# Optimization experiments

Measured on AMD Instinct MI355X. Metric: run time of the kernel, lower is better.

The kernel has to match this reference:

```python
import jax, jax.numpy as jnp
import numpy as np

DIM = 1024          # hidden_size
HEADS = 16
KDIM = DIM // 2     # expand_k = 0.5
VDIM = DIM          # expand_v = 1.0
DK = KDIM // HEADS  # 32 head key dim
DV = VDIM // HEADS  # 64 head value dim
LOW = 16            # gate_low_rank_dim
NORMALIZER = 16.0   # gate_logit_normalizer
EPS = 1e-5
B, T = 2, 4096


def setup_inputs() -> dict:
    key = jax.random.key(0)
    ks = jax.random.split(key, 9)
    def lin(k, sh, fan_in):
        return jax.random.normal(k, sh, jnp.float32) * (fan_in ** -0.5)
    return {
        "x":    jax.random.normal(ks[0], (B, T, DIM), jnp.float32),
        "Wq":   lin(ks[1], (DIM, KDIM), DIM),
        "Wk":   lin(ks[2], (DIM, KDIM), DIM),
        "Wv":   lin(ks[3], (DIM, VDIM), DIM),
        "Wgk1": lin(ks[4], (DIM, LOW), DIM),   # low-rank gate proj (no bias)
        "Wgk2": lin(ks[5], (LOW, KDIM), LOW),  # low-rank gate proj (with bias)
        "bgk2": jnp.zeros((KDIM,), jnp.float32),
        "Wg":   lin(ks[6], (DIM, VDIM), DIM),  # output gate proj (no bias)
        "gnw":  jnp.ones((DV,), jnp.float32),  # per-head RMSNorm weight
        "Wo":   lin(ks[7], (VDIM, DIM), VDIM),
    }


def _gla_scan(q, k, v, gk):
    # q,k,gk: (B,T,H,DK)  v: (B,T,H,DV)
    # recurrent form of chunked GLA: h_t = exp(gk_t) (x) h_{t-1} + k_t (outer) v_t
    scale = DK ** -0.5
    def step(h, inp):
        qt, kt, vt, gt = inp                      # (B,H,DK)/(B,H,DV)
        h = h * jnp.exp(gt)[..., None] + kt[..., None] * vt[..., None, :]
        ot = jnp.einsum('bhk,bhkv->bhv', qt * scale, h)
        return h, ot
    h0 = jnp.zeros((q.shape[0], HEADS, DK, DV), q.dtype)
    xs = tuple(jnp.moveaxis(a, 1, 0) for a in (q, k, v, gk))  # time-major
    _, o = jax.lax.scan(step, h0, xs)
    return jnp.moveaxis(o, 0, 1)                  # (B,T,H,DV)


def reference(x, Wq, Wk, Wv, Wgk1, Wgk2, bgk2, Wg, gnw, Wo):
    Bx, Tx, _ = x.shape
    q = (x @ Wq).reshape(Bx, Tx, HEADS, DK)
    k = (x @ Wk).reshape(Bx, Tx, HEADS, DK)
    v = (x @ Wv).reshape(Bx, Tx, HEADS, DV)
    # data-dependent log-decay gate: logsigmoid(low-rank proj) / normalizer
    gk = jax.nn.log_sigmoid((x @ Wgk1) @ Wgk2 + bgk2)
    gk = gk.reshape(Bx, Tx, HEADS, DK) / NORMALIZER
    o = _gla_scan(q, k, v, gk)                    # (B,T,H,DV)
    # fused per-head RMSNorm + swish output gate
    g = (x @ Wg).reshape(Bx, Tx, HEADS, DV)
    o = o * jax.lax.rsqrt(jnp.mean(o * o, axis=-1, keepdims=True) + EPS) * gnw
    o = o * (g * jax.nn.sigmoid(g))
    return o.reshape(Bx, Tx, VDIM) @ Wo
```

## Files before the change

### kernel.cpp

```cpp
#include <hip/hip_runtime.h>

typedef unsigned short u16;
typedef unsigned int u32;
typedef __attribute__((ext_vector_type(8))) short short8;
typedef __attribute__((ext_vector_type(4))) float f32x4;

#define KD 512
#define HEADS 16
#define DK 32
#define DV 64
#define TT 4096
#define MROWS 8192
#define CHUNK 64
#define NCH 64
#define NBH 32
#define QSTR 3328
#define SCALE 0.17677669529663687f

__device__ __forceinline__ u16 f2bf(float f) {
    union { float f; unsigned int u; } x; x.f = f;
    unsigned int u = x.u;
    unsigned int r = (u + 0x7fffu + ((u >> 16) & 1u)) >> 16;
    return (u16)r;
}
__device__ __forceinline__ float bf2f(u16 s) {
    union { unsigned int u; float f; } x; x.u = ((unsigned int)s) << 16;
    return x.f;
}
__device__ __forceinline__ void gload16(const u16* g, u16* l) {
    __builtin_amdgcn_global_load_lds((const __attribute__((address_space(1))) u32*)g,
                                     (__attribute__((address_space(3))) u32*)l, 16, 0, 0);
}

__global__ __launch_bounds__(256) void f32_to_bf16_vec(const float* __restrict__ src,
                                                       u16* __restrict__ dst, int n4) {
    int i = blockIdx.x * 256 + threadIdx.x;
    if (i < n4) {
        const float4 v = ((const float4*)src)[i];
        ushort4 o;
        o.x = f2bf(v.x); o.y = f2bf(v.y); o.z = f2bf(v.z); o.w = f2bf(v.w);
        ((ushort4*)dst)[i] = o;
    }
}

__global__ __launch_bounds__(256) void weight_prep(const float* __restrict__ Wq,
                                                   const float* __restrict__ Wk,
                                                   const float* __restrict__ Wv,
                                                   const float* __restrict__ Wg,
                                                   const float* __restrict__ W1,
                                                   const float* __restrict__ Wo,
                                                   u16* __restrict__ dst) {
    __shared__ float tile[32][33];
    int n0 = blockIdx.x * 32, k0 = blockIdx.y * 32;
    int tx = threadIdx.x & 31, ty = threadIdx.x >> 5;
    int n = n0 + tx;
    const float* src; int sN, cc;
    if (n < 512)       { src = Wq; sN = 512;  cc = n; }
    else if (n < 1024) { src = Wk; sN = 512;  cc = n - 512; }
    else if (n < 2048) { src = Wv; sN = 1024; cc = n - 1024; }
    else if (n < 3072) { src = Wg; sN = 1024; cc = n - 2048; }
    else if (n < 3088) { src = W1; sN = 16;   cc = n - 3072; }
    else if (n < 3328) { src = nullptr; sN = 0; cc = 0; }
    else               { src = Wo; sN = 1024; cc = n - 3328; }
    for (int r = ty; r < 32; r += 8)
        tile[r][tx] = src ? src[(size_t)(k0 + r) * sN + cc] : 0.f;
    __syncthreads();
    for (int r = ty; r < 32; r += 8)
        dst[(size_t)(n0 + r) * 1024 + k0 + tx] = f2bf(tile[tx][r]);
}

#define BARM() do { asm volatile("" ::: "memory"); __builtin_amdgcn_s_barrier(); asm volatile("" ::: "memory"); } while (0)
#define VMW(n) asm volatile("s_waitcnt vmcnt(" #n ")" ::: "memory")

template<int OUTBF>
__global__ __launch_bounds__(512, 2) void gemm8(const u16* __restrict__ A,
                                                const u16* __restrict__ Bt,
                                                void* __restrict__ C,
                                                int M, int N, int K, int nbx) {
    __shared__ u16 SA[2][16384];
    __shared__ u16 SB[2][16384];
    int nwg = gridDim.x, bid = blockIdx.x, cpx = nwg >> 3;
    int wg = (bid & 7) * cpx + (bid >> 3);
    int bx = wg % nbx, by = wg / nbx;
    int brow = by << 8, bcol = bx << 8;
    int tid = threadIdx.x;
    int wv = tid >> 6, lane = tid & 63;
    int wm = wv >> 2, wn = wv & 3;
    int l15 = lane & 15, hi = lane >> 4;
    int rxor = l15 & 7;

    int srw = tid >> 3;
    int sg8 = ((tid & 7) ^ (srw & 7)) << 3;
    const u16* aBase = A + (size_t)(brow + srw) * K + sg8;
    const u16* bBase = Bt + (size_t)(bcol + ((tid >> 8) << 6) + (srw & 31)) * K + sg8;

#define STAGE_A(b, h, tt) do { \
        const u16* s_ = aBase + (size_t)(tt) * 64 + (size_t)(h) * 64 * K; \
        gload16(s_,                    &SA[b][(h) * 8192 + tid * 8]); \
        gload16(s_ + (size_t)128 * K,  &SA[b][(h) * 8192 + 4096 + tid * 8]); \
    } while (0)
#define STAGE_B(b, h, tt) do { \
        const u16* s_ = bBase + (size_t)(tt) * 64 + (size_t)(h) * 32 * K; \
        gload16(s_,                    &SB[b][(h) * 8192 + tid * 8]); \
        gload16(s_ + (size_t)128 * K,  &SB[b][(h) * 8192 + 4096 + tid * 8]); \
    } while (0)

    int aRow = (wm * 64 + l15) * 64;
    int bRow = (wn * 32 + l15) * 64;
    int cg0 = (hi ^ rxor) << 3;
    int cg1 = ((4 + hi) ^ rxor) << 3;

#define READ_A(dst, mh, b) do { \
        _Pragma("unroll") \
        for (int mil_ = 0; mil_ < 4; ++mil_) { \
            dst[mil_ * 2 + 0] = *(const short8*)&SA[b][(mh) * 8192 + mil_ * 1024 + aRow + cg0]; \
            dst[mil_ * 2 + 1] = *(const short8*)&SA[b][(mh) * 8192 + mil_ * 1024 + aRow + cg1]; \
        } } while (0)
#define READ_B(dst, nh, b) do { \
        _Pragma("unroll") \
        for (int nil_ = 0; nil_ < 2; ++nil_) { \
            dst[nil_ * 2 + 0] = *(const short8*)&SB[b][(nh) * 8192 + nil_ * 1024 + bRow + cg0]; \
            dst[nil_ * 2 + 1] = *(const short8*)&SB[b][(nh) * 8192 + nil_ * 1024 + bRow + cg1]; \
        } } while (0)

    f32x4 acc[8][4];
    #pragma unroll
    for (int mi = 0; mi < 8; ++mi)
        #pragma unroll
        for (int ni = 0; ni < 4; ++ni)
            acc[mi][ni] = (f32x4){0.f, 0.f, 0.f, 0.f};

#define MM(mb, nb, AF, BF) do { \
        __builtin_amdgcn_s_setprio(1); \
        _Pragma("unroll") \
        for (int ks_ = 0; ks_ < 2; ++ks_) \
        _Pragma("unroll") \
        for (int mil_ = 0; mil_ < 4; ++mil_) \
        _Pragma("unroll") \
        for (int nil_ = 0; nil_ < 2; ++nil_) \
            acc[(mb) + mil_][(nb) + nil_] = __builtin_amdgcn_mfma_f32_16x16x32_bf16( \
                AF[mil_ * 2 + ks_], BF[nil_ * 2 + ks_], acc[(mb) + mil_][(nb) + nil_], 0, 0, 0); \
        __builtin_amdgcn_s_setprio(0); \
    } while (0)

    int NK = K >> 6, NI = NK >> 1;
    STAGE_B(0, 0, 0); STAGE_A(0, 0, 0); STAGE_A(0, 1, 0); STAGE_B(0, 1, 0);
    STAGE_B(1, 0, 1); STAGE_A(1, 0, 1); STAGE_A(1, 1, 1);
    VMW(6);
    BARM();

    short8 alo[8], ahi[8], bb[4];
    for (int i = 0; i < NI; ++i) {
        int ta = 2 * i + 1; if (ta >= NK) ta = NK - 1;
        int tb = 2 * i + 2; if (tb >= NK) tb = NK - 1;
        int tc = 2 * i + 3; if (tc >= NK) tc = NK - 1;
        STAGE_B(1, 1, ta);
        READ_A(alo, 0, 0); READ_B(bb, 0, 0);
        BARM(); MM(0, 0, alo, bb); BARM();
        STAGE_B(0, 0, tb);
        READ_A(ahi, 1, 0);
        BARM(); MM(4, 0, ahi, bb); BARM();
        STAGE_A(0, 0, tb); STAGE_A(0, 1, tb);
        READ_B(bb, 1, 0);
        BARM(); MM(4, 2, ahi, bb); MM(0, 2, alo, bb);
        VMW(8);
        BARM();
        STAGE_B(0, 1, tb);
        READ_A(alo, 0, 1); READ_B(bb, 0, 1);
        BARM(); MM(0, 0, alo, bb); BARM();
        STAGE_B(1, 0, tc);
        READ_A(ahi, 1, 1);
        BARM(); MM(4, 0, ahi, bb);
        VMW(10);
        BARM();
        STAGE_A(1, 0, tc); STAGE_A(1, 1, tc);
        READ_B(bb, 1, 1);
        BARM(); MM(4, 2, ahi, bb); MM(0, 2, alo, bb);
        VMW(6);
        BARM();
    }

    int r0 = brow + wm * 128 + (hi << 2);
    int c0 = bcol + wn * 64 + l15;
    #pragma unroll
    for (int mi = 0; mi < 8; ++mi)
        #pragma unroll
        for (int ni = 0; ni < 4; ++ni)
            #pragma unroll
            for (int rr = 0; rr < 4; ++rr) {
                size_t idx = (size_t)(r0 + mi * 16 + rr) * N + (c0 + ni * 16);
                float val = acc[mi][ni][rr];
                if (OUTBF) ((u16*)C)[idx] = f2bf(val);
                else       ((float*)C)[idx] = val;
            }
#undef STAGE_A
#undef STAGE_B
#undef READ_A
#undef READ_B
#undef MM
}

template<int OUTBF>
__global__ __launch_bounds__(256) void gemm_sb(const u16* __restrict__ A,
                                               const u16* __restrict__ Bt,
                                               void* __restrict__ C,
                                               int M, int N, int K, int nbx) {
    __shared__ u16 As[128 * 64];
    __shared__ u16 Bs[128 * 64];
    int nwg = gridDim.x;
    int bid = blockIdx.x;
    int cpx = nwg >> 3;
    int wg = (bid & 7) * cpx + (bid >> 3);
    int bx = wg % nbx, by = wg / nbx;
    int tid = threadIdx.x;
    int wave = tid >> 6, lane = tid & 63;
    int wr = wave >> 1, wc = wave & 1;
    int brow = by * 128, bcol = bx * 128;
    int srow = tid >> 3;
    int sgrp = (tid & 7) ^ (srow & 7);
    const u16* aS = A + (size_t)(brow + srow) * K + sgrp * 8;
    const u16* bS = Bt + (size_t)(bcol + srow) * K + sgrp * 8;
    f32x4 acc[4][4];
    #pragma unroll
    for (int mi = 0; mi < 4; ++mi)
        #pragma unroll
        for (int ni = 0; ni < 4; ++ni)
            acc[mi][ni] = (f32x4){0.f, 0.f, 0.f, 0.f};
    int l15 = lane & 15, hi = lane >> 4;
    int rxor = l15 & 7;
    for (int kt = 0; kt < K; kt += 64) {
        __syncthreads();
        #pragma unroll
        for (int i_ = 0; i_ < 4; ++i_) {
            gload16(aS + (size_t)i_ * 32 * K + kt, As + tid * 8 + i_ * 2048);
            gload16(bS + (size_t)i_ * 32 * K + kt, Bs + tid * 8 + i_ * 2048);
        }
        __syncthreads();
        #pragma unroll
        for (int ks = 0; ks < 2; ++ks) {
            short8 af[4], bfr[4];
            int g = ks * 4 + hi;
            #pragma unroll
            for (int i = 0; i < 4; ++i)
                af[i] = *(const short8*)(As + (size_t)(wr * 64 + i * 16 + l15) * 64 + ((g ^ rxor) << 3));
            #pragma unroll
            for (int i = 0; i < 4; ++i)
                bfr[i] = *(const short8*)(Bs + (size_t)(wc * 64 + i * 16 + l15) * 64 + ((g ^ rxor) << 3));
            #pragma unroll
            for (int mi = 0; mi < 4; ++mi)
                #pragma unroll
                for (int ni = 0; ni < 4; ++ni)
                    acc[mi][ni] = __builtin_amdgcn_mfma_f32_16x16x32_bf16(af[mi], bfr[ni], acc[mi][ni], 0, 0, 0);
        }
    }
    int r0 = brow + wr * 64 + (hi << 2);
    int c0 = bcol + wc * 64 + l15;
    #pragma unroll
    for (int mi = 0; mi < 4; ++mi)
        #pragma unroll
        for (int ni = 0; ni < 4; ++ni)
            #pragma unroll
            for (int rr = 0; rr < 4; ++rr) {
                size_t idx = (size_t)(r0 + mi * 16 + rr) * N + (c0 + ni * 16);
                float val = acc[mi][ni][rr];
                if (OUTBF) ((u16*)C)[idx] = f2bf(val);
                else       ((float*)C)[idx] = val;
            }
}

__device__ __forceinline__ void gate_z8(const u16* __restrict__ xg,
                                        const float* __restrict__ W2,
                                        const float* __restrict__ b2,
                                        int cc, float* out8) {
    short8 x0 = *(const short8*)xg;
    short8 x1 = *(const short8*)(xg + 8);
    float z[8];
    float4 z0 = *(const float4*)(b2 + cc);
    float4 z1 = *(const float4*)(b2 + cc + 4);
    z[0]=z0.x; z[1]=z0.y; z[2]=z0.z; z[3]=z0.w;
    z[4]=z1.x; z[5]=z1.y; z[6]=z1.z; z[7]=z1.w;
    #pragma unroll
    for (int u = 0; u < 16; ++u) {
        float xu = bf2f((u16)(u < 8 ? x0[u] : x1[u - 8]));
        const float4 w0 = *(const float4*)(W2 + (size_t)u * 512 + cc);
        const float4 w1 = *(const float4*)(W2 + (size_t)u * 512 + cc + 4);
        z[0] += xu * w0.x; z[1] += xu * w0.y; z[2] += xu * w0.z; z[3] += xu * w0.w;
        z[4] += xu * w1.x; z[5] += xu * w1.y; z[6] += xu * w1.z; z[7] += xu * w1.w;
    }
    #pragma unroll
    for (int j = 0; j < 8; ++j) {
        float zz = z[j];
        out8[j] = (fminf(zz, 0.f) - log1pf(expf(-fabsf(zz)))) * 0.0625f;
    }
}

__global__ __launch_bounds__(256) void phaseA(const u16* __restrict__ qkvg,
                                              const float* __restrict__ W2,
                                              const float* __restrict__ b2,
                                              float* __restrict__ MT_ws,
                                              float* __restrict__ D_ws) {
    int bh = blockIdx.x >> 6, c = blockIdx.x & 63;
    int b = bh >> 4, h = bh & 15;
    int t0 = b * TT + c * CHUNK;
    __shared__ float gkS[64][36];
    __shared__ u16 kdT_bf[32 * 72];
    __shared__ u16 VT_bf[64 * 72];
    __shared__ float Z[32];
    int tid = threadIdx.x;
    int s = tid >> 2, i0 = (tid & 3) << 3;
    {
        float ls[8];
        gate_z8(qkvg + (size_t)(t0 + s) * QSTR + 3072, W2, b2, h * DK + i0, ls);
        #pragma unroll
        for (int jj = 0; jj < 8; ++jj) gkS[s][i0 + jj] = ls[jj];
    }
    short8 kv = *(const short8*)(qkvg + (size_t)(t0 + s) * QSTR + 512 + h * DK + i0);
    {
        int j0 = (tid & 3) << 4;
        short8 v0 = *(const short8*)(qkvg + (size_t)(t0 + s) * QSTR + 1024 + h * DV + j0);
        short8 v1 = *(const short8*)(qkvg + (size_t)(t0 + s) * QSTR + 1024 + h * DV + j0 + 8);
        #pragma unroll
        for (int jj = 0; jj < 8; ++jj) {
            VT_bf[(j0 + jj) * 72 + s] = (u16)v0[jj];
            VT_bf[(j0 + 8 + jj) * 72 + s] = (u16)v1[jj];
        }
    }
    __syncthreads();
    if (tid < 32) {
        float run = 0.f;
        for (int t = 0; t < 64; ++t) { run += gkS[t][tid]; gkS[t][tid] = run; }
        Z[tid] = run;
    }
    __syncthreads();
    #pragma unroll
    for (int jj = 0; jj < 8; ++jj)
        kdT_bf[(i0 + jj) * 72 + s] = f2bf(expf(Z[i0 + jj] - gkS[s][i0 + jj]) * bf2f((u16)kv[jj]));
    __syncthreads();
    int wave = tid >> 6, lane = tid & 63, l15 = lane & 15, hi = lane >> 4;
    int it = wave & 1, jp = wave >> 1;
    size_t base = ((size_t)(bh * NCH + c)) * 2048;
    #pragma unroll
    for (int jj2 = 0; jj2 < 2; ++jj2) {
        int jt = jp * 2 + jj2;
        f32x4 mc = (f32x4){0.f, 0.f, 0.f, 0.f};
        #pragma unroll
        for (int kc = 0; kc < 2; ++kc) {
            short8 ak = *(const short8*)&kdT_bf[(it * 16 + l15) * 72 + kc * 32 + hi * 8];
            short8 bv = *(const short8*)&VT_bf[(jt * 16 + l15) * 72 + kc * 32 + hi * 8];
            mc = __builtin_amdgcn_mfma_f32_16x16x32_bf16(ak, bv, mc, 0, 0, 0);
        }
        #pragma unroll
        for (int rr = 0; rr < 4; ++rr)
            MT_ws[base + (size_t)(jt * 16 + l15) * 32 + it * 16 + hi * 4 + rr] = mc[rr];
    }
    if (tid < 32) D_ws[(size_t)(bh * NCH + c) * 32 + tid] = expf(Z[tid]);
}

__global__ __launch_bounds__(256) void phaseB(const float* __restrict__ MT_ws,
                                              const float* __restrict__ D_ws,
                                              float* __restrict__ HT_ws) {
    int idx = blockIdx.x * 256 + threadIdx.x;
    int bh = idx >> 11;
    int ji = idx & 2047;
    int i = ji & 31;
    float h = 0.f;
    size_t base = (size_t)bh * NCH * 2048 + ji;
    const float* dp = D_ws + (size_t)bh * NCH * 32 + i;
    for (int c = 0; c < NCH; ++c) {
        HT_ws[base + (size_t)c * 2048] = h;
        h = h * dp[c * 32] + MT_ws[base + (size_t)c * 2048];
    }
}

__global__ __launch_bounds__(256) void phaseC(const u16* __restrict__ qkvg,
                                              const float* __restrict__ W2,
                                              const float* __restrict__ b2,
                                              const float* __restrict__ HT_ws,
                                              const float* __restrict__ gnw,
                                              u16* __restrict__ o_n) {
    int bh = blockIdx.x >> 6, c = blockIdx.x & 63;
    int b = bh >> 4, h = bh & 15;
    int t0 = b * TT + c * CHUNK;
    __shared__ float gkS[64][36];
    __shared__ u16 qh_bf[64 * 40];
    __shared__ u16 kt_bf[64 * 40];
    __shared__ u16 VT_bf[64 * 72];
    __shared__ u16 Ht_bf[64 * 40];
    u16* P_bf = (u16*)&gkS[0][0];
    int tid = threadIdx.x;
    int s = tid >> 2, i0 = (tid & 3) << 3;
    {
        float ls[8];
        gate_z8(qkvg + (size_t)(t0 + s) * QSTR + 3072, W2, b2, h * DK + i0, ls);
        #pragma unroll
        for (int jj = 0; jj < 8; ++jj) gkS[s][i0 + jj] = ls[jj];
    }
    short8 qv = *(const short8*)(qkvg + (size_t)(t0 + s) * QSTR + h * DK + i0);
    short8 kv = *(const short8*)(qkvg + (size_t)(t0 + s) * QSTR + 512 + h * DK + i0);
    {
        int j0 = (tid & 3) << 4;
        short8 v0 = *(const short8*)(qkvg + (size_t)(t0 + s) * QSTR + 1024 + h * DV + j0);
        short8 v1 = *(const short8*)(qkvg + (size_t)(t0 + s) * QSTR + 1024 + h * DV + j0 + 8);
        #pragma unroll
        for (int jj = 0; jj < 8; ++jj) {
            VT_bf[(j0 + jj) * 72 + s] = (u16)v0[jj];
            VT_bf[(j0 + 8 + jj) * 72 + s] = (u16)v1[jj];
        }
    }
    {
        const float* hp = HT_ws + ((size_t)(bh * NCH + c)) * 2048 + tid * 8;
        float4 h0 = *(const float4*)hp;
        float4 h1 = *(const float4*)(hp + 4);
        int j = tid >> 2, ii0 = (tid & 3) << 3;
        ushort4 o0, o1;
        o0.x = f2bf(h0.x); o0.y = f2bf(h0.y); o0.z = f2bf(h0.z); o0.w = f2bf(h0.w);
        o1.x = f2bf(h1.x); o1.y = f2bf(h1.y); o1.z = f2bf(h1.z); o1.w = f2bf(h1.w);
        *(ushort4*)&Ht_bf[j * 40 + ii0] = o0;
        *(ushort4*)&Ht_bf[j * 40 + ii0 + 4] = o1;
    }
    __syncthreads();
    if (tid < 32) {
        float run = 0.f;
        for (int t = 0; t < 64; ++t) { run += gkS[t][tid]; gkS[t][tid] = run; }
    }
    __syncthreads();
    #pragma unroll
    for (int jj = 0; jj < 8; ++jj) {
        float Sv = gkS[s][i0 + jj];
        qh_bf[s * 40 + i0 + jj] = f2bf(bf2f((u16)qv[jj]) * expf(Sv) * SCALE);
        kt_bf[s * 40 + i0 + jj] = f2bf(bf2f((u16)kv[jj]) * expf(fminf(-Sv, 80.f)));
    }
    __syncthreads();
    int wave = tid >> 6, lane = tid & 63, l15 = lane & 15, hi = lane >> 4;
    int w = wave;
    short8 aq = *(const short8*)&qh_bf[(w * 16 + l15) * 40 + hi * 8];
    #pragma unroll
    for (int sn = 0; sn < 4; ++sn) {
        f32x4 sc = (f32x4){0.f, 0.f, 0.f, 0.f};
        if (sn <= w) {
            short8 bk = *(const short8*)&kt_bf[(sn * 16 + l15) * 40 + hi * 8];
            sc = __builtin_amdgcn_mfma_f32_16x16x32_bf16(aq, bk, sc, 0, 0, 0);
        }
        #pragma unroll
        for (int rr = 0; rr < 4; ++rr) {
            float val = sc[rr];
            if (sn > w || (sn == w && l15 > hi * 4 + rr)) val = 0.f;
            P_bf[(w * 16 + hi * 4 + rr) * 72 + sn * 16 + l15] = f2bf(val);
        }
    }
    __syncthreads();
    f32x4 acc[4];
    #pragma unroll
    for (int jn = 0; jn < 4; ++jn) {
        f32x4 a = (f32x4){0.f, 0.f, 0.f, 0.f};
        short8 bhf = *(const short8*)&Ht_bf[(jn * 16 + l15) * 40 + hi * 8];
        acc[jn] = __builtin_amdgcn_mfma_f32_16x16x32_bf16(aq, bhf, a, 0, 0, 0);
    }
    int nkc = (w < 2) ? 1 : 2;
    for (int kc = 0; kc < nkc; ++kc) {
        short8 ap = *(const short8*)&P_bf[(w * 16 + l15) * 72 + kc * 32 + hi * 8];
        #pragma unroll
        for (int jn = 0; jn < 4; ++jn) {
            short8 bv = *(const short8*)&VT_bf[(jn * 16 + l15) * 72 + kc * 32 + hi * 8];
            acc[jn] = __builtin_amdgcn_mfma_f32_16x16x32_bf16(ap, bv, acc[jn], 0, 0, 0);
        }
    }
    #pragma unroll
    for (int rr = 0; rr < 4; ++rr) {
        float sum2 = 0.f;
        #pragma unroll
        for (int jn = 0; jn < 4; ++jn) sum2 += acc[jn][rr] * acc[jn][rr];
        sum2 += __shfl_xor(sum2, 1);
        sum2 += __shfl_xor(sum2, 2);
        sum2 += __shfl_xor(sum2, 4);
        sum2 += __shfl_xor(sum2, 8);
        float rms = rsqrtf(sum2 * (1.f / 64.f) + 1e-5f);
        int t = w * 16 + hi * 4 + rr;
        #pragma unroll
        for (int jn = 0; jn < 4; ++jn) {
            int j = jn * 16 + l15;
            float g = bf2f(qkvg[(size_t)(t0 + t) * QSTR + 2048 + h * DV + j]);
            float sw = g / (1.f + expf(-g));
            float o = acc[jn][rr] * rms * gnw[j] * sw;
            o_n[(size_t)(t0 + t) * 1024 + h * DV + j] = f2bf(o);
        }
    }
}

extern "C" void kernel_launch(void* const* d_in, const int* in_sizes, int n_in,
                              void* d_out, int out_size, void* d_ws, size_t ws_size,
                              hipStream_t stream) {
    const float* x    = (const float*)d_in[0];
    const float* Wq   = (const float*)d_in[1];
    const float* Wk   = (const float*)d_in[2];
    const float* Wv   = (const float*)d_in[3];
    const float* Wgk1 = (const float*)d_in[4];
    const float* Wgk2 = (const float*)d_in[5];
    const float* bgk2 = (const float*)d_in[6];
    const float* Wg   = (const float*)d_in[7];
    const float* gnw  = (const float*)d_in[8];
    const float* Wo   = (const float*)d_in[9];

    char* ws = (char*)d_ws;
    size_t off = 0;
    u16* xb      = (u16*)(ws + off); off += (size_t)MROWS * 1024 * 2;
    u16* Wall    = (u16*)(ws + off); off += (size_t)4352 * 1024 * 2;
    u16* qkvg    = (u16*)(ws + off); off += (size_t)MROWS * QSTR * 2;
    float* MT_ws = (float*)(ws + off); off += (size_t)NBH * NCH * 2048 * 4;
    float* D_ws  = (float*)(ws + off); off += (size_t)NBH * NCH * 32 * 4;
    float* HT_ws = (float*)(ws + off); off += (size_t)NBH * NCH * 2048 * 4;
    u16* o_n     = (u16*)(ws + off); off += (size_t)MROWS * 1024 * 2;
    u16* WcatT   = Wall;
    u16* WoT     = Wall + (size_t)3328 * 1024;

    f32_to_bf16_vec<<<MROWS, 256, 0, stream>>>(x, xb, MROWS * 1024 / 4);
    weight_prep<<<dim3(136, 32), 256, 0, stream>>>(Wq, Wk, Wv, Wg, Wgk1, Wo, Wall);
    gemm8<1><<<416, 512, 0, stream>>>(xb, WcatT, qkvg, MROWS, QSTR, 1024, 13);
    phaseA<<<NBH * NCH, 256, 0, stream>>>(qkvg, Wgk2, bgk2, MT_ws, D_ws);
    phaseB<<<256, 256, 0, stream>>>(MT_ws, D_ws, HT_ws);
    phaseC<<<NBH * NCH, 256, 0, stream>>>(qkvg, Wgk2, bgk2, HT_ws, gnw, o_n);
    gemm_sb<0><<<8 * 64, 256, 0, stream>>>(o_n, WoT, d_out, MROWS, 1024, 1024, 8);
}
```

Before: 174.0 us.

## Fuse prep kernels, store chunk states in bf16, parallelize gate cumsum

Merges the x-to-bf16 conversion and weight transpose into a single launch. Stores the per-chunk state matrices MT and HT as bf16 instead of fp32, halving workspace traffic in phaseA/B/C and removing the conversion in phaseC. Replaces the 32-thread serial 64-step cumulative sum of gate logits with a wave-level shuffle scan over all 256 threads. The bf16 MT storage adds rounding before the inter-chunk recurrence, which may slightly reduce accuracy.

```diff
diff --git a/kernel.cpp b/kernel.cpp
--- a/kernel.cpp
+++ b/kernel.cpp
@@ -32,26 +32,27 @@
                                      (__attribute__((address_space(3))) u32*)l, 16, 0, 0);
 }
 
-__global__ __launch_bounds__(256) void f32_to_bf16_vec(const float* __restrict__ src,
-                                                       u16* __restrict__ dst, int n4) {
-    int i = blockIdx.x * 256 + threadIdx.x;
-    if (i < n4) {
-        const float4 v = ((const float4*)src)[i];
+__global__ __launch_bounds__(256) void prep_fused(const float* __restrict__ x,
+                                                  u16* __restrict__ xb,
+                                                  const float* __restrict__ Wq,
+                                                  const float* __restrict__ Wk,
+                                                  const float* __restrict__ Wv,
+                                                  const float* __restrict__ Wg,
+                                                  const float* __restrict__ W1,
+                                                  const float* __restrict__ Wo,
+                                                  u16* __restrict__ dst) {
+    __shared__ float tile[32][33];
+    int bid = blockIdx.x;
+    if (bid < 8192) {
+        int i = bid * 256 + threadIdx.x;
+        const float4 v = ((const float4*)x)[i];
         ushort4 o;
         o.x = f2bf(v.x); o.y = f2bf(v.y); o.z = f2bf(v.z); o.w = f2bf(v.w);
-        ((ushort4*)dst)[i] = o;
-    }
-}
-
-__global__ __launch_bounds__(256) void weight_prep(const float* __restrict__ Wq,
-                                                   const float* __restrict__ Wk,
-                                                   const float* __restrict__ Wv,
-                                                   const float* __restrict__ Wg,
-                                                   const float* __restrict__ W1,
-                                                   const float* __restrict__ Wo,
-                                                   u16* __restrict__ dst) {
-    __shared__ float tile[32][33];
-    int n0 = blockIdx.x * 32, k0 = blockIdx.y * 32;
+        ((ushort4*)xb)[i] = o;
+        return;
+    }
+    int w = bid - 8192;
+    int n0 = (w % 136) * 32, k0 = (w / 136) * 32;
     int tx = threadIdx.x & 31, ty = threadIdx.x >> 5;
     int n = n0 + tx;
     const float* src; int sN, cc;
@@ -294,10 +295,26 @@
     }
 }
 
+__device__ __forceinline__ void scan64(float (*gkS)[36], float* Ztot, int tid) {
+    int wv2 = tid >> 6, ln = tid & 63;
+    #pragma unroll
+    for (int ii = 0; ii < 8; ++ii) {
+        int i = wv2 * 8 + ii;
+        float v = gkS[ln][i];
+        #pragma unroll
+        for (int d = 1; d < 64; d <<= 1) {
+            float u = __shfl_up(v, d);
+            if (ln >= d) v += u;
+        }
+        gkS[ln][i] = v;
+        if (Ztot && ln == 63) Ztot[i] = v;
+    }
+}
+
 __global__ __launch_bounds__(256) void phaseA(const u16* __restrict__ qkvg,
                                               const float* __restrict__ W2,
                                               const float* __restrict__ b2,
-                                              float* __restrict__ MT_ws,
+                                              u16* __restrict__ MT_ws,
                                               float* __restrict__ D_ws) {
     int bh = blockIdx.x >> 6, c = blockIdx.x & 63;
     int b = bh >> 4, h = bh & 15;
@@ -326,11 +343,7 @@
         }
     }
     __syncthreads();
-    if (tid < 32) {
-        float run = 0.f;
-        for (int t = 0; t < 64; ++t) { run += gkS[t][tid]; gkS[t][tid] = run; }
-        Z[tid] = run;
-    }
+    scan64(gkS, Z, tid);
     __syncthreads();
     #pragma unroll
     for (int jj = 0; jj < 8; ++jj)
@@ -351,14 +364,14 @@
         }
         #pragma unroll
         for (int rr = 0; rr < 4; ++rr)
-            MT_ws[base + (size_t)(jt * 16 + l15) * 32 + it * 16 + hi * 4 + rr] = mc[rr];
+            MT_ws[base + (size_t)(jt * 16 + l15) * 32 + it * 16 + hi * 4 + rr] = f2bf(mc[rr]);
     }
     if (tid < 32) D_ws[(size_t)(bh * NCH + c) * 32 + tid] = expf(Z[tid]);
 }
 
-__global__ __launch_bounds__(256) void phaseB(const float* __restrict__ MT_ws,
+__global__ __launch_bounds__(256) void phaseB(const u16* __restrict__ MT_ws,
                                               const float* __restrict__ D_ws,
-                                              float* __restrict__ HT_ws) {
+                                              u16* __restrict__ HT_ws) {
     int idx = blockIdx.x * 256 + threadIdx.x;
     int bh = idx >> 11;
     int ji = idx & 2047;
@@ -367,15 +380,15 @@
     size_t base = (size_t)bh * NCH * 2048 + ji;
     const float* dp = D_ws + (size_t)bh * NCH * 32 + i;
     for (int c = 0; c < NCH; ++c) {
-        HT_ws[base + (size_t)c * 2048] = h;
-        h = h * dp[c * 32] + MT_ws[base + (size_t)c * 2048];
+        HT_ws[base + (size_t)c * 2048] = f2bf(h);
+        h = h * dp[c * 32] + bf2f(MT_ws[base + (size_t)c * 2048]);
     }
 }
 
 __global__ __launch_bounds__(256) void phaseC(const u16* __restrict__ qkvg,
                                               const float* __restrict__ W2,
                                               const float* __restrict__ b2,
-                                              const float* __restrict__ HT_ws,
+                                              const u16* __restrict__ HT_ws,
                                               const float* __restrict__ gnw,
                                               u16* __restrict__ o_n) {
     int bh = blockIdx.x >> 6, c = blockIdx.x & 63;
@@ -408,21 +421,13 @@
         }
     }
     {
-        const float* hp = HT_ws + ((size_t)(bh * NCH + c)) * 2048 + tid * 8;
-        float4 h0 = *(const float4*)hp;
-        float4 h1 = *(const float4*)(hp + 4);
+        const u16* hp = HT_ws + ((size_t)(bh * NCH + c)) * 2048 + tid * 8;
+        short8 hv = *(const short8*)hp;
         int j = tid >> 2, ii0 = (tid & 3) << 3;
-        ushort4 o0, o1;
-        o0.x = f2bf(h0.x); o0.y = f2bf(h0.y); o0.z = f2bf(h0.z); o0.w = f2bf(h0.w);
-        o1.x = f2bf(h1.x); o1.y = f2bf(h1.y); o1.z = f2bf(h1.z); o1.w = f2bf(h1.w);
-        *(ushort4*)&Ht_bf[j * 40 + ii0] = o0;
-        *(ushort4*)&Ht_bf[j * 40 + ii0 + 4] = o1;
-    }
-    __syncthreads();
-    if (tid < 32) {
-        float run = 0.f;
-        for (int t = 0; t < 64; ++t) { run += gkS[t][tid]; gkS[t][tid] = run; }
-    }
+        *(short8*)&Ht_bf[j * 40 + ii0] = hv;
+    }
+    __syncthreads();
+    scan64(gkS, nullptr, tid);
     __syncthreads();
     #pragma unroll
     for (int jj = 0; jj < 8; ++jj) {
@@ -506,15 +511,14 @@
     u16* xb      = (u16*)(ws + off); off += (size_t)MROWS * 1024 * 2;
     u16* Wall    = (u16*)(ws + off); off += (size_t)4352 * 1024 * 2;
     u16* qkvg    = (u16*)(ws + off); off += (size_t)MROWS * QSTR * 2;
-    float* MT_ws = (float*)(ws + off); off += (size_t)NBH * NCH * 2048 * 4;
+    u16* MT_ws   = (u16*)(ws + off); off += (size_t)NBH * NCH * 2048 * 2;
     float* D_ws  = (float*)(ws + off); off += (size_t)NBH * NCH * 32 * 4;
-    float* HT_ws = (float*)(ws + off); off += (size_t)NBH * NCH * 2048 * 4;
+    u16* HT_ws   = (u16*)(ws + off); off += (size_t)NBH * NCH * 2048 * 2;
     u16* o_n     = (u16*)(ws + off); off += (size_t)MROWS * 1024 * 2;
     u16* WcatT   = Wall;
     u16* WoT     = Wall + (size_t)3328 * 1024;
 
-    f32_to_bf16_vec<<<MROWS, 256, 0, stream>>>(x, xb, MROWS * 1024 / 4);
-    weight_prep<<<dim3(136, 32), 256, 0, stream>>>(Wq, Wk, Wv, Wg, Wgk1, Wo, Wall);
+    prep_fused<<<8192 + 136 * 32, 256, 0, stream>>>(x, xb, Wq, Wk, Wv, Wg, Wgk1, Wo, Wall);
     gemm8<1><<<416, 512, 0, stream>>>(xb, WcatT, qkvg, MROWS, QSTR, 1024, 13);
     phaseA<<<NBH * NCH, 256, 0, stream>>>(qkvg, Wgk2, bgk2, MT_ws, D_ws);
     phaseB<<<256, 256, 0, stream>>>(MT_ws, D_ws, HT_ws);
```

Measured after the change: 173.5 us. About the same (-0.3%).
